# Optimization experiments

Measured on AMD Instinct MI355X. Metric: run time of the kernel, lower is better.

The kernel has to match this reference:

```python
import jax, jax.numpy as jnp
import numpy as np

EMBEDDING_LOSS_WEIGHT = 1.0
COMMITMENT_LOSS_WEIGHT = 0.25
ENTROPY_LOSS_WEIGHT = 0.02


def setup_inputs() -> dict:
    key = jax.random.key(0)
    k1, k2 = jax.random.split(key)
    inputs = jax.random.normal(k1, (16, 32, 32, 256), dtype=jnp.float32)
    # RandomUniform() default range in keras is [-0.05, 0.05]
    codebook = jax.random.uniform(k2, (4096, 256), dtype=jnp.float32,
                                  minval=-0.05, maxval=0.05)
    return {"inputs": inputs, "codebook": codebook}


def reference(inputs, codebook):
    sg = jax.lax.stop_gradient
    B, H, W, D = inputs.shape
    K = codebook.shape[0]
    flat = inputs.reshape(-1, D)  # [N, D], N = B*H*W

    x_sq = jnp.sum(flat * flat, axis=-1, keepdims=True)          # [N, 1]
    c_sq = jnp.sum(codebook * codebook, axis=-1)                 # [K]
    cross = flat @ codebook.T                                    # [N, K] GEMM
    distances = x_sq + c_sq - 2.0 * cross                        # [N, K]

    tokens = jnp.argmin(distances, axis=-1)                      # [N] int32
    embeddings = jnp.take(codebook, tokens, axis=0).reshape(B, H, W, D)

    embedding_loss = EMBEDDING_LOSS_WEIGHT * jnp.mean((sg(embeddings) - inputs) ** 2)
    commitment_loss = COMMITMENT_LOSS_WEIGHT * jnp.mean((embeddings - sg(inputs)) ** 2)

    # entropy loss: for codebook entries never selected, penalize their
    # minimum distance to any input vector
    active = jnp.zeros((K,), jnp.int32).at[tokens].add(1)        # scatter counts
    min_dist_per_class = jnp.min(distances, axis=0)              # [K]
    entropy_loss = ENTROPY_LOSS_WEIGHT * jnp.mean(
        jnp.where(active == 0, min_dist_per_class, 0.0))

    loss = embedding_loss + commitment_loss + entropy_loss

    # training=True straight-through estimator
    out = inputs + sg(embeddings - inputs)
    return out, loss
```

## Files before the change

### kernel.cpp

```cpp
#include <hip/hip_runtime.h>
#include <stdint.h>


#define N_ROWS 16384
#define DIM    256
#define KCODES 4096
#define NCHUNK 8
#define KC     (KCODES / NCHUNK)
#define TM     128
#define TN     128
#define BK     32
#define NKT    (KC / TN)
#define NDC    (DIM / BK)
#define NSTEP  (NKT * NDC)
#define NGRAN  (NCHUNK * 2)
#define NRB    (N_ROWS / TM)

typedef float    f32x4 __attribute__((ext_vector_type(4)));
typedef _Float16 f16x8 __attribute__((ext_vector_type(8)));

#define GLOAD_LDS16(g, l) __builtin_amdgcn_global_load_lds(                 \
    (const __attribute__((address_space(1))) void*)(g),                     \
    (__attribute__((address_space(3))) void*)(l), 16, 0, 0)

__device__ __forceinline__ unsigned umin_(unsigned a, unsigned b) { return a < b ? a : b; }
__device__ __forceinline__ unsigned umax_(unsigned a, unsigned b) { return a > b ? a : b; }
__device__ __forceinline__ unsigned long long umin64_(unsigned long long a,
                                                      unsigned long long b) {
    return a < b ? a : b;
}
__device__ __forceinline__ unsigned long long umax64_(unsigned long long a,
                                                      unsigned long long b) {
    return a > b ? a : b;
}

__device__ __forceinline__ unsigned fkey(float f) {
    unsigned b = __float_as_uint(f);
    return (b & 0x80000000u) ? ~b : (b | 0x80000000u);
}
__device__ __forceinline__ float fkey_inv(unsigned k) {
    unsigned b = (k & 0x80000000u) ? (k ^ 0x80000000u) : ~k;
    return __uint_as_float(b);
}
__device__ __forceinline__ unsigned short f2h(float f) {
    union { _Float16 h; unsigned short u; } cv;
    cv.h = (_Float16)f;
    return cv.u;
}

__global__ __launch_bounds__(256) void vq_prep_kernel(
        const float* __restrict__ x, const float* __restrict__ cb,
        unsigned short* __restrict__ xh, unsigned short* __restrict__ ch,
        float* __restrict__ xsq, float* __restrict__ csq,
        unsigned* __restrict__ active, double* __restrict__ accum,
        unsigned* __restrict__ counter) {
    const int b = blockIdx.x, t = threadIdx.x;
    if (b < KCODES / 256) {
        int i = b * 256 + t;
        active[i] = 0u;
        if (i == 0) { accum[0] = 0.0; accum[1] = 0.0; counter[0] = 0u; }
    }
    const size_t NX = (size_t)N_ROWS * DIM;
    size_t e = (size_t)b * 1024 + (size_t)t * 4;
    const float* src; unsigned short* dst; float* sq; size_t off;
    if (e < NX) { src = x;  dst = xh; sq = xsq; off = e; }
    else        { src = cb; dst = ch; sq = csq; off = e - NX; }
    float4 v = *(const float4*)(src + off);
    ushort4 h;
    h.x = f2h(v.x); h.y = f2h(v.y); h.z = f2h(v.z); h.w = f2h(v.w);
    *(ushort4*)(dst + off) = h;
    double s = (double)v.x * v.x + (double)v.y * v.y
             + (double)v.z * v.z + (double)v.w * v.w;
    for (int o = 32; o; o >>= 1) s += __shfl_down(s, o);
    if ((t & 63) == 0) sq[off >> 8] = (float)s;
}

__global__ __launch_bounds__(256, 2) void vq_gemm_kernel(
        const unsigned short* __restrict__ xh_g, const unsigned short* __restrict__ ch_g,
        const float* __restrict__ xsq, const float* __restrict__ csq,
        unsigned* __restrict__ colmin_part, uint2* __restrict__ top2_out) {
    __shared__ __align__(16) unsigned short b_lds[2][TN][BK];
    __shared__ float    xsq_l[128];
    __shared__ unsigned colmin_l[KC];
    __shared__ uint2    u12_l[16][256];

    const int t = threadIdx.x;
    const int wave = t >> 6, lane = t & 63, quad = lane >> 4, L = lane & 15;
    const int whalf = wave >> 1, chalf = wave & 1;
    const int row0  = blockIdx.x * TM;
    const int code0 = blockIdx.y * KC;

    if (t < 128) xsq_l[t] = xsq[row0 + t];
    colmin_l[t] = 0xFFFFFFFFu; colmin_l[t + 256] = 0xFFFFFFFFu;
#pragma unroll
    for (int i = 0; i < 16; ++i)
        u12_l[i][t] = make_uint2(0xFFFFFFFFu, 0xFFFFFFFFu);

    const unsigned short* abase =
        xh_g + ((size_t)(row0 + whalf * 64 + L) * DIM + quad * 8);

    auto stageB = [&](int buf, int kt_, int dc_) {
        const unsigned short* bsrc =
            ch_g + (size_t)(code0 + kt_ * TN) * DIM + dc_ * BK;
        unsigned short* dst = &b_lds[buf][0][0];
#pragma unroll
        for (int k = 0; k < 2; ++k) {
            const int j = t + k * 256;
            const int r = j >> 2, sg = (j & 3) ^ ((j >> 3) & 3);
            GLOAD_LDS16(bsrc + (size_t)r * DIM + sg * 8, dst + (size_t)j * 8);
        }
    };

    const int bslot = (L >> 1) & 3;

    stageB(0, 0, 0);
    f16x8 afr[NDC][4];
#pragma unroll
    for (int dc = 0; dc < NDC; ++dc)
#pragma unroll
        for (int mt = 0; mt < 4; ++mt)
            afr[dc][mt] = *(const f16x8*)(abase + (size_t)mt * 16 * DIM + dc * BK);

    for (int kt = 0; kt < NKT; ++kt) {
        const int cb0 = code0 + kt * TN;
        f32x4 acc[4][4];
#pragma unroll
        for (int mt = 0; mt < 4; ++mt)
#pragma unroll
            for (int nt = 0; nt < 4; ++nt) acc[mt][nt] = (f32x4){0.f, 0.f, 0.f, 0.f};

#pragma unroll
        for (int dc = 0; dc < NDC; ++dc) {
            const int cur = dc & 1;
            __syncthreads();
            if (!(kt == NKT - 1 && dc == NDC - 1))
                stageB(cur ^ 1, kt + (dc == NDC - 1), (dc + 1) & 7);

            f16x8 bf[4];
#pragma unroll
            for (int nt = 0; nt < 4; ++nt)
                bf[nt] = *(const f16x8*)
                    &b_lds[cur][chalf * 64 + nt * 16 + L][(quad ^ bslot) * 8];
#pragma unroll
            for (int mt = 0; mt < 4; ++mt)
#pragma unroll
                for (int nt = 0; nt < 4; ++nt)
                    acc[mt][nt] = __builtin_amdgcn_mfma_f32_16x16x32_f16(
                        afr[dc][mt], bf[nt], acc[mt][nt], 0, 0, 0);
        }

        float csq4[4]; unsigned colf[4];
        float dmin[4] = {3.4e38f, 3.4e38f, 3.4e38f, 3.4e38f};
#pragma unroll
        for (int nt = 0; nt < 4; ++nt) {
            csq4[nt] = csq[cb0 + chalf * 64 + nt * 16 + L];
            colf[nt] = (unsigned)(kt * 128 + chalf * 64 + nt * 16 + L);
        }
#pragma unroll
        for (int mt = 0; mt < 4; ++mt) {
            const f32x4 xq = *(const f32x4*)&xsq_l[whalf * 64 + mt * 16 + quad * 4];
#pragma unroll
            for (int reg = 0; reg < 4; ++reg) {
                const int i = mt * 4 + reg;
                uint2 e = u12_l[i][t];
#pragma unroll
                for (int nt = 0; nt < 4; ++nt) {
                    float s = fmaf(-2.0f, acc[mt][nt][reg], csq4[nt]);
                    unsigned key = (fkey(s) & 0xFFFFFE00u) | colf[nt];
                    unsigned lo = umin_(e.x, key);
                    e.y = umin_(e.y, umax_(e.x, key));
                    e.x = lo;
                    dmin[nt] = fminf(dmin[nt], xq[reg] + s);
                }
                u12_l[i][t] = e;
            }
        }
#pragma unroll
        for (int nt = 0; nt < 4; ++nt) {
            unsigned dk = fkey(dmin[nt]);
            dk = umin_(dk, (unsigned)__shfl_xor((int)dk, 16));
            dk = umin_(dk, (unsigned)__shfl_xor((int)dk, 32));
            if (quad == 0)
                atomicMin(&colmin_l[kt * TN + chalf * 64 + nt * 16 + L], dk);
        }
    }

    unsigned u1[16], u2[16];
#pragma unroll
    for (int i = 0; i < 16; ++i) {
        uint2 e = u12_l[i][t];
        u1[i] = e.x; u2[i] = e.y;
    }
#pragma unroll
    for (int i = 0; i < 16; ++i) {
#pragma unroll
        for (int st = 1; st < 16; st <<= 1) {
            unsigned w1 = (unsigned)__shfl_xor((int)u1[i], st);
            unsigned w2 = (unsigned)__shfl_xor((int)u2[i], st);
            unsigned a = umin_(u1[i], w1), b = umax_(u1[i], w1);
            u1[i] = a;
            u2[i] = umin_(umin_(u2[i], w2), b);
        }
    }
    if (L == 0) {
        const size_t gbase = (size_t)(blockIdx.y * 2 + chalf) * N_ROWS;
#pragma unroll
        for (int mt = 0; mt < 4; ++mt)
#pragma unroll
            for (int reg = 0; reg < 4; ++reg) {
                const int row = row0 + whalf * 64 + mt * 16 + quad * 4 + reg;
                top2_out[gbase + row] = make_uint2(u1[mt * 4 + reg], u2[mt * 4 + reg]);
            }
    }

    __syncthreads();
    unsigned* cp = colmin_part + (size_t)blockIdx.x * KCODES + code0;
    cp[t]       = colmin_l[t];
    cp[t + 256] = colmin_l[t + 256];
}

__global__ __launch_bounds__(256) void vq_refine_kernel(
        const float* __restrict__ x, const float* __restrict__ cb,
        const uint2* __restrict__ top2, unsigned* __restrict__ active,
        float* __restrict__ out, double* __restrict__ accum) {
    __shared__ double wsum[4];
    const int wave = threadIdx.x >> 6, lane = threadIdx.x & 63;
    const int row  = blockIdx.x * 4 + wave;

    const int g = (lane >> 1) & 15;
    uint2 e = top2[(size_t)g * N_ROWS + row];
    unsigned key = (lane & 1) ? e.y : e.x;
    unsigned idc = (unsigned)((g >> 1) * KC) + (key & 0x1FFu);
    unsigned long long pk =
        ((unsigned long long)(key & 0xFFFFFE00u) << 32) | idc;
    if (lane >= 32) pk = ~0ull;

    unsigned long long m1 = pk, m2 = ~0ull;
#pragma unroll
    for (int o = 1; o < 64; o <<= 1) {
        unsigned long long w1 = (unsigned long long)__shfl_xor((long long)m1, o);
        unsigned long long w2 = (unsigned long long)__shfl_xor((long long)m2, o);
        unsigned long long lo = umin64_(m1, w1), hi = umax64_(m1, w1);
        m1 = lo;
        m2 = umin64_(umin64_(m2, w2), hi);
    }
    const float v0 = fkey_inv((unsigned)(m1 >> 32));
    const float v1 = fkey_inv((unsigned)(m2 >> 32));

    float4 xv = ((const float4*)(x + (size_t)row * DIM))[lane];
    int tok;
    if (v1 > v0 + 1.0e-2f) {
        tok = (int)(unsigned)(m1 & 0xFFFFFFFFu);
    } else {
        int id8[8];
        unsigned long long cur = pk;
#pragma unroll
        for (int k = 0; k < 8; ++k) {
            unsigned long long m = cur;
#pragma unroll
            for (int o = 1; o < 64; o <<= 1)
                m = umin64_(m, (unsigned long long)__shfl_xor((long long)m, o));
            id8[k] = (int)(unsigned)(m & 0xFFFFFFFFu);
            if (cur == m) cur = ~0ull;
        }

        double xs64 = (double)xv.x * xv.x + (double)xv.y * xv.y
                    + (double)xv.z * xv.z + (double)xv.w * xv.w;
        double dd[8], cc2[8];
#pragma unroll
        for (int k = 0; k < 8; ++k) {
            float4 c4 = ((const float4*)(cb + (size_t)id8[k] * DIM))[lane];
            dd[k]  = (double)xv.x * c4.x + (double)xv.y * c4.y
                   + (double)xv.z * c4.z + (double)xv.w * c4.w;
            cc2[k] = (double)c4.x * c4.x + (double)c4.y * c4.y
                   + (double)c4.z * c4.z + (double)c4.w * c4.w;
        }
#pragma unroll
        for (int o = 32; o; o >>= 1) {
            xs64 += __shfl_down(xs64, o);
#pragma unroll
            for (int k = 0; k < 8; ++k) {
                dd[k]  += __shfl_down(dd[k], o);
                cc2[k] += __shfl_down(cc2[k], o);
            }
        }
        if (lane == 0) {
            double D[8], Dmin = 1e300;
#pragma unroll
            for (int k = 0; k < 8; ++k) {
                D[k] = xs64 + cc2[k] - 2.0 * dd[k];
                Dmin = fmin(Dmin, D[k]);
            }
            int e2; frexp(Dmin, &e2);
            double U   = ldexp(1.0, e2 - 1 - 23);
            double thr = Dmin + 0.75 * U;
            tok = 0x7FFFFFFF;
#pragma unroll
            for (int k = 0; k < 8; ++k)
                if (D[k] <= thr && id8[k] < tok) tok = id8[k];
        }
        tok = __shfl(tok, 0);
    }

    if (lane == 0) active[tok] = 1u;
    float4 sel = ((const float4*)(cb + (size_t)tok * DIM))[lane];
    ((float4*)out)[(size_t)row * 64 + lane] = sel;
    float dx = sel.x - xv.x, dy = sel.y - xv.y, dz = sel.z - xv.z, dw = sel.w - xv.w;
    float s = dx * dx + dy * dy + dz * dz + dw * dw;
    for (int o = 32; o; o >>= 1) s += __shfl_down(s, o);
    if (lane == 0) wsum[wave] = (double)s;
    __syncthreads();
    if (threadIdx.x == 0) atomicAdd(accum, wsum[0] + wsum[1] + wsum[2] + wsum[3]);
}

__global__ __launch_bounds__(256) void vq_final_kernel(
        const unsigned* __restrict__ colmin_part, const unsigned* __restrict__ active,
        double* __restrict__ accum, unsigned* __restrict__ counter,
        float* __restrict__ out) {
    __shared__ double red[256];
    const int t = threadIdx.x;
    const int c = blockIdx.x * 256 + t;
    unsigned m = 0xFFFFFFFFu;
#pragma unroll 8
    for (int rb = 0; rb < NRB; ++rb)
        m = umin_(m, colmin_part[(size_t)rb * KCODES + c]);
    red[t] = (active[c] == 0u) ? (double)fkey_inv(m) : 0.0;
    __syncthreads();
    for (int o = 128; o; o >>= 1) {
        if (t < o) red[t] += red[t + o];
        __syncthreads();
    }
    if (t == 0) {
        atomicAdd(&accum[1], red[0]);
        __threadfence();
        unsigned old = atomicAdd(counter, 1u);
        if (old == 15u) {
            __threadfence();
            double ent = atomicAdd(&accum[1], 0.0);
            double loss = 1.25 * (accum[0] / (double)((size_t)N_ROWS * DIM))
                        + 0.02 * (ent / (double)KCODES);
            out[(size_t)N_ROWS * DIM] = (float)loss;
        }
    }
}

extern "C" void kernel_launch(void* const* d_in, const int* in_sizes, int n_in,
                              void* d_out, int out_size, void* d_ws, size_t ws_size,
                              hipStream_t stream) {
    const float* x  = (const float*)d_in[0];
    const float* cb = (const float*)d_in[1];
    float* out = (float*)d_out;

    char* ws = (char*)d_ws;
    float*    xsq     = (float*)(ws + 0);
    float*    csq     = (float*)(ws + 65536);
    unsigned* active  = (unsigned*)(ws + 81920);
    double*   accum   = (double*)(ws + 98304);
    unsigned* counter = (unsigned*)(ws + 98560);
    uint2*    top2    = (uint2*)(ws + 131072);
    unsigned* cpart   = (unsigned*)(ws + 2228224);
    unsigned short* xh_g = (unsigned short*)(ws + 4325376);
    unsigned short* ch_g = (unsigned short*)(ws + 12713984);

    vq_prep_kernel<<<((N_ROWS + KCODES) * DIM) / 1024, 256, 0, stream>>>(
        x, cb, xh_g, ch_g, xsq, csq, active, accum, counter);
    vq_gemm_kernel<<<dim3(NRB, NCHUNK), 256, 0, stream>>>(
        xh_g, ch_g, xsq, csq, cpart, top2);
    vq_refine_kernel<<<N_ROWS / 4, 256, 0, stream>>>(
        x, cb, top2, active, out, accum);
    vq_final_kernel<<<KCODES / 256, 256, 0, stream>>>(
        cpart, active, accum, counter, out);
}
```

Baseline: 203.0 us.

## Deepen B-tile LDS pipeline to four buffers with explicit vmcnt waits

```diff
diff --git a/kernel.cpp b/kernel.cpp
--- a/kernel.cpp
+++ b/kernel.cpp
@@ -23,6 +23,8 @@
     (const __attribute__((address_space(1))) void*)(g),                     \
     (__attribute__((address_space(3))) void*)(l), 16, 0, 0)
 
+#define WAITVM(n) asm volatile("s_waitcnt vmcnt(" #n ")" ::: "memory")
+
 __device__ __forceinline__ unsigned umin_(unsigned a, unsigned b) { return a < b ? a : b; }
 __device__ __forceinline__ unsigned umax_(unsigned a, unsigned b) { return a > b ? a : b; }
 __device__ __forceinline__ unsigned long long umin64_(unsigned long long a,
@@ -79,7 +81,7 @@
         const unsigned short* __restrict__ xh_g, const unsigned short* __restrict__ ch_g,
         const float* __restrict__ xsq, const float* __restrict__ csq,
         unsigned* __restrict__ colmin_part, uint2* __restrict__ top2_out) {
-    __shared__ __align__(16) unsigned short b_lds[2][TN][BK];
+    __shared__ __align__(16) unsigned short b_lds[4][TN][BK];
     __shared__ float    xsq_l[128];
     __shared__ unsigned colmin_l[KC];
     __shared__ uint2    u12_l[16][256];
@@ -113,16 +115,24 @@
 
     const int bslot = (L >> 1) & 3;
 
-    stageB(0, 0, 0);
     f16x8 afr[NDC][4];
 #pragma unroll
     for (int dc = 0; dc < NDC; ++dc)
 #pragma unroll
         for (int mt = 0; mt < 4; ++mt)
             afr[dc][mt] = *(const f16x8*)(abase + (size_t)mt * 16 * DIM + dc * BK);
-
+    float csq_r[NKT][4];
+#pragma unroll
+    for (int kt = 0; kt < NKT; ++kt)
+#pragma unroll
+        for (int nt = 0; nt < 4; ++nt)
+            csq_r[kt][nt] = csq[code0 + kt * TN + chalf * 64 + nt * 16 + L];
+    stageB(0, 0, 0);
+    stageB(1, 0, 1);
+    stageB(2, 0, 2);
+
+#pragma unroll
     for (int kt = 0; kt < NKT; ++kt) {
-        const int cb0 = code0 + kt * TN;
         f32x4 acc[4][4];
 #pragma unroll
         for (int mt = 0; mt < 4; ++mt)
@@ -131,16 +141,20 @@
 
 #pragma unroll
         for (int dc = 0; dc < NDC; ++dc) {
-            const int cur = dc & 1;
-            __syncthreads();
-            if (!(kt == NKT - 1 && dc == NDC - 1))
-                stageB(cur ^ 1, kt + (dc == NDC - 1), (dc + 1) & 7);
+            const int s = kt * NDC + dc;
+            if (s < NSTEP - 2)      WAITVM(4);
+            else if (s == NSTEP - 2) WAITVM(2);
+            else                     WAITVM(0);
+            __builtin_amdgcn_s_barrier();
+            __builtin_amdgcn_sched_barrier(0);
+            if (s + 3 < NSTEP)
+                stageB((s + 3) & 3, (s + 3) >> 3, (s + 3) & 7);
 
             f16x8 bf[4];
 #pragma unroll
             for (int nt = 0; nt < 4; ++nt)
                 bf[nt] = *(const f16x8*)
-                    &b_lds[cur][chalf * 64 + nt * 16 + L][(quad ^ bslot) * 8];
+                    &b_lds[s & 3][chalf * 64 + nt * 16 + L][(quad ^ bslot) * 8];
 #pragma unroll
             for (int mt = 0; mt < 4; ++mt)
 #pragma unroll
@@ -149,13 +163,11 @@
                         afr[dc][mt], bf[nt], acc[mt][nt], 0, 0, 0);
         }
 
-        float csq4[4]; unsigned colf[4];
+        unsigned colf[4];
         float dmin[4] = {3.4e38f, 3.4e38f, 3.4e38f, 3.4e38f};
 #pragma unroll
-        for (int nt = 0; nt < 4; ++nt) {
-            csq4[nt] = csq[cb0 + chalf * 64 + nt * 16 + L];
+        for (int nt = 0; nt < 4; ++nt)
             colf[nt] = (unsigned)(kt * 128 + chalf * 64 + nt * 16 + L);
-        }
 #pragma unroll
         for (int mt = 0; mt < 4; ++mt) {
             const f32x4 xq = *(const f32x4*)&xsq_l[whalf * 64 + mt * 16 + quad * 4];
@@ -165,7 +177,7 @@
                 uint2 e = u12_l[i][t];
 #pragma unroll
                 for (int nt = 0; nt < 4; ++nt) {
-                    float s = fmaf(-2.0f, acc[mt][nt][reg], csq4[nt]);
+                    float s = fmaf(-2.0f, acc[mt][nt][reg], csq_r[kt][nt]);
                     unsigned key = (fkey(s) & 0xFFFFFE00u) | colf[nt];
                     unsigned lo = umin_(e.x, key);
                     e.y = umin_(e.y, umax_(e.x, key));
```

Result: slower. 213.2 us (+5.0%).

## Deepen codebook LDS pipeline to four buffers with vmcnt-based waits

Applied to the files above, without the earlier changes.

```diff
diff --git a/kernel.cpp b/kernel.cpp
--- a/kernel.cpp
+++ b/kernel.cpp
@@ -23,6 +23,10 @@
     (const __attribute__((address_space(1))) void*)(g),                     \
     (__attribute__((address_space(3))) void*)(l), 16, 0, 0)
 
+#define WAITVM_(n) asm volatile("s_waitcnt vmcnt(" #n ")" ::: "memory")
+#define WAITVM(n)  WAITVM_(n)
+#define MEMPIN()   asm volatile("" ::: "memory")
+
 __device__ __forceinline__ unsigned umin_(unsigned a, unsigned b) { return a < b ? a : b; }
 __device__ __forceinline__ unsigned umax_(unsigned a, unsigned b) { return a > b ? a : b; }
 __device__ __forceinline__ unsigned long long umin64_(unsigned long long a,
@@ -79,8 +83,9 @@
         const unsigned short* __restrict__ xh_g, const unsigned short* __restrict__ ch_g,
         const float* __restrict__ xsq, const float* __restrict__ csq,
         unsigned* __restrict__ colmin_part, uint2* __restrict__ top2_out) {
-    __shared__ __align__(16) unsigned short b_lds[2][TN][BK];
+    __shared__ __align__(16) unsigned short b_lds[4][TN][BK];
     __shared__ float    xsq_l[128];
+    __shared__ float    csq_l[KC];
     __shared__ unsigned colmin_l[KC];
     __shared__ uint2    u12_l[16][256];
 
@@ -91,6 +96,8 @@
     const int code0 = blockIdx.y * KC;
 
     if (t < 128) xsq_l[t] = xsq[row0 + t];
+    csq_l[t]       = csq[code0 + t];
+    csq_l[t + 256] = csq[code0 + t + 256];
     colmin_l[t] = 0xFFFFFFFFu; colmin_l[t + 256] = 0xFFFFFFFFu;
 #pragma unroll
     for (int i = 0; i < 16; ++i)
@@ -113,47 +120,30 @@
 
     const int bslot = (L >> 1) & 3;
 
-    stageB(0, 0, 0);
     f16x8 afr[NDC][4];
 #pragma unroll
     for (int dc = 0; dc < NDC; ++dc)
 #pragma unroll
         for (int mt = 0; mt < 4; ++mt)
             afr[dc][mt] = *(const f16x8*)(abase + (size_t)mt * 16 * DIM + dc * BK);
-
-    for (int kt = 0; kt < NKT; ++kt) {
-        const int cb0 = code0 + kt * TN;
-        f32x4 acc[4][4];
-#pragma unroll
-        for (int mt = 0; mt < 4; ++mt)
-#pragma unroll
-            for (int nt = 0; nt < 4; ++nt) acc[mt][nt] = (f32x4){0.f, 0.f, 0.f, 0.f};
-
-#pragma unroll
-        for (int dc = 0; dc < NDC; ++dc) {
-            const int cur = dc & 1;
-            __syncthreads();
-            if (!(kt == NKT - 1 && dc == NDC - 1))
-                stageB(cur ^ 1, kt + (dc == NDC - 1), (dc + 1) & 7);
-
-            f16x8 bf[4];
-#pragma unroll
-            for (int nt = 0; nt < 4; ++nt)
-                bf[nt] = *(const f16x8*)
-                    &b_lds[cur][chalf * 64 + nt * 16 + L][(quad ^ bslot) * 8];
-#pragma unroll
-            for (int mt = 0; mt < 4; ++mt)
-#pragma unroll
-                for (int nt = 0; nt < 4; ++nt)
-                    acc[mt][nt] = __builtin_amdgcn_mfma_f32_16x16x32_f16(
-                        afr[dc][mt], bf[nt], acc[mt][nt], 0, 0, 0);
-        }
-
+    MEMPIN();
+    stageB(0, 0, 0);
+    MEMPIN();
+    stageB(1, 0, 1);
+    MEMPIN();
+    stageB(2, 0, 2);
+    MEMPIN();
+
+    asm volatile("s_waitcnt lgkmcnt(0)" ::: "memory");
+    __builtin_amdgcn_s_barrier();
+    __builtin_amdgcn_sched_barrier(0);
+
+    auto epilogue = [&](int kt, f32x4 (&acc)[4][4]) {
         float csq4[4]; unsigned colf[4];
         float dmin[4] = {3.4e38f, 3.4e38f, 3.4e38f, 3.4e38f};
 #pragma unroll
         for (int nt = 0; nt < 4; ++nt) {
-            csq4[nt] = csq[cb0 + chalf * 64 + nt * 16 + L];
+            csq4[nt] = csq_l[kt * TN + chalf * 64 + nt * 16 + L];
             colf[nt] = (unsigned)(kt * 128 + chalf * 64 + nt * 16 + L);
         }
 #pragma unroll
@@ -183,6 +173,33 @@
             if (quad == 0)
                 atomicMin(&colmin_l[kt * TN + chalf * 64 + nt * 16 + L], dk);
         }
+    };
+
+    for (int kt = 0; kt < NKT; ++kt) {
+        f32x4 acc[4][4];
+#pragma unroll
+        for (int mt = 0; mt < 4; ++mt)
+#pragma unroll
+            for (int nt = 0; nt < 4; ++nt) acc[mt][nt] = (f32x4){0.f, 0.f, 0.f, 0.f};
+#pragma unroll
+        for (int dc = 0; dc < NDC; ++dc) {
+            WAITVM(4);
+            __builtin_amdgcn_s_barrier();
+            __builtin_amdgcn_sched_barrier(0);
+            stageB((dc + 3) & 3, (kt + (dc >= 5)) & 3, (dc + 3) & 7);
+            f16x8 bf[4];
+#pragma unroll
+            for (int nt = 0; nt < 4; ++nt)
+                bf[nt] = *(const f16x8*)
+                    &b_lds[dc & 3][chalf * 64 + nt * 16 + L][(quad ^ bslot) * 8];
+#pragma unroll
+            for (int mt = 0; mt < 4; ++mt)
+#pragma unroll
+                for (int nt = 0; nt < 4; ++nt)
+                    acc[mt][nt] = __builtin_amdgcn_mfma_f32_16x16x32_f16(
+                        afr[dc][mt], bf[nt], acc[mt][nt], 0, 0, 0);
+        }
+        epilogue(kt, acc);
     }
 
     unsigned u1[16], u2[16];
@@ -266,29 +283,28 @@
 
         double xs64 = (double)xv.x * xv.x + (double)xv.y * xv.y
                     + (double)xv.z * xv.z + (double)xv.w * xv.w;
-        double dd[8], cc2[8];
+        double p[8];
 #pragma unroll
         for (int k = 0; k < 8; ++k) {
             float4 c4 = ((const float4*)(cb + (size_t)id8[k] * DIM))[lane];
-            dd[k]  = (double)xv.x * c4.x + (double)xv.y * c4.y
-                   + (double)xv.z * c4.z + (double)xv.w * c4.w;
-            cc2[k] = (double)c4.x * c4.x + (double)c4.y * c4.y
-                   + (double)c4.z * c4.z + (double)c4.w * c4.w;
+            double dd  = (double)xv.x * c4.x + (double)xv.y * c4.y
+                       + (double)xv.z * c4.z + (double)xv.w * c4.w;
+            double cc2 = (double)c4.x * c4.x + (double)c4.y * c4.y
+                       + (double)c4.z * c4.z + (double)c4.w * c4.w;
+            p[k] = cc2 - 2.0 * dd;
         }
 #pragma unroll
         for (int o = 32; o; o >>= 1) {
             xs64 += __shfl_down(xs64, o);
 #pragma unroll
-            for (int k = 0; k < 8; ++k) {
-                dd[k]  += __shfl_down(dd[k], o);
-                cc2[k] += __shfl_down(cc2[k], o);
-            }
+            for (int k = 0; k < 8; ++k)
+                p[k] += __shfl_down(p[k], o);
         }
         if (lane == 0) {
             double D[8], Dmin = 1e300;
 #pragma unroll
             for (int k = 0; k < 8; ++k) {
-                D[k] = xs64 + cc2[k] - 2.0 * dd[k];
+                D[k] = xs64 + p[k];
                 Dmin = fmin(Dmin, D[k]);
             }
             int e2; frexp(Dmin, &e2);
```

Result: no change. 204.0 us (+0.5%).
